# Performance work log

Hardware: AMD Instinct MI355X
Metric: run time of the kernel (lower is better)

The kernel has to match this reference:

```python
import jax, jax.numpy as jnp
import numpy as np

B, S, D = 2, 2048, 1024
H, DH = 16, 64  # num_heads, qk/vo embed size per head
NEG_INF = -1e9


def setup_inputs() -> dict:
    key = jax.random.key(0)
    ks = jax.random.split(key, 7)
    return {
        "query": jax.random.normal(ks[0], (B, S, D), jnp.float32),
        "key": jax.random.normal(ks[1], (B, S, D), jnp.float32),
        "value": jax.random.normal(ks[2], (B, S, D), jnp.float32),
        "Wq": jax.random.normal(ks[3], (D, D), jnp.float32) * 0.02,
        "Wk": jax.random.normal(ks[4], (D, D), jnp.float32) * 0.02,
        "Wv": jax.random.normal(ks[5], (D, D), jnp.float32) * 0.02,
        "Wo": jax.random.normal(ks[6], (D, D), jnp.float32) * 0.02,
    }


def reference(query, key, value, Wq, Wk, Wv, Wo):
    # projections (nn.Linear, no bias): y = x @ W.T
    q = (query @ Wq.T).reshape(B, S, H, DH)
    k = (key @ Wk.T).reshape(B, S, H, DH)
    v = (value @ Wv.T).reshape(B, S, H, DH)
    # scores normalized by sqrt(per-head qk embed dim)
    scores = jnp.einsum("bqhd,bkhd->bhqk", q, k) / jnp.sqrt(jnp.float32(DH))
    # causal mask
    causal = jnp.tril(jnp.ones((S, S), dtype=bool))
    scores = jnp.where(causal[None, None, :, :], scores, NEG_INF)
    attn = jax.nn.softmax(scores, axis=-1)  # attention_type='softmax'
    ctx = jnp.einsum("bhqk,bkhd->bqhd", attn, v).reshape(B, S, H * DH)
    return ctx @ Wo.T
```

## Files before the change

### kernel.cpp

```cpp
#include <hip/hip_runtime.h>
#include <hip/hip_bf16.h>
#include <cstdint>


typedef __attribute__((ext_vector_type(8))) __bf16 bf16x8;
typedef __attribute__((ext_vector_type(8))) unsigned short ushort8;
typedef __attribute__((ext_vector_type(4))) unsigned short usv4;
typedef __attribute__((ext_vector_type(4))) float f32x4;
typedef unsigned short ushort_t;

#define B_ 2
#define S_ 2048
#define D_ 1024
#define H_ 16
#define DH_ 64
#define BK 64

#define QSCALE 0.1803368801111244f

__device__ __forceinline__ ushort_t f2b(float f) {
  uint32_t u = __builtin_bit_cast(uint32_t, f);
  u += 0x7fffu + ((u >> 16) & 1u);
  return (ushort_t)(u >> 16);
}
__device__ __forceinline__ ushort_t f2bf(float f) {
  uint32_t u = __builtin_bit_cast(uint32_t, f);
  return (ushort_t)((u + 0x8000u) >> 16);
}

__device__ __forceinline__ f32x4 mfma16(bf16x8 a, bf16x8 b, f32x4 c) {
  return __builtin_amdgcn_mfma_f32_16x16x32_bf16(a, b, c, 0, 0, 0);
}

__device__ __forceinline__ void gload16(const ushort_t* g, char* lds) {
  __builtin_amdgcn_global_load_lds(
      (__attribute__((address_space(1))) void*)(uintptr_t)g,
      (__attribute__((address_space(3))) void*)(uintptr_t)lds, 16, 0, 0);
}

__global__ __launch_bounds__(256) void cvt3_kernel(
    const float* __restrict__ s0, const float* __restrict__ s1,
    const float* __restrict__ s2, ushort_t* __restrict__ d0,
    ushort_t* __restrict__ d1, ushort_t* __restrict__ d2) {
  const float* src = blockIdx.y == 0 ? s0 : (blockIdx.y == 1 ? s1 : s2);
  ushort_t* dst = blockIdx.y == 0 ? d0 : (blockIdx.y == 1 ? d1 : d2);
  int i = blockIdx.x * 256 + threadIdx.x;
  f32x4 a = ((const f32x4*)src)[i * 2];
  f32x4 b = ((const f32x4*)src)[i * 2 + 1];
  ushort8 o;
#pragma unroll
  for (int j = 0; j < 4; ++j) o[j] = f2b(a[j]);
#pragma unroll
  for (int j = 0; j < 4; ++j) o[4 + j] = f2b(b[j]);
  ((ushort8*)dst)[i] = o;
}

__global__ __launch_bounds__(256) void cvt4_kernel(
    const float* __restrict__ s0, const float* __restrict__ s1,
    const float* __restrict__ s2, const float* __restrict__ s3,
    ushort_t* __restrict__ d0, ushort_t* __restrict__ d1,
    ushort_t* __restrict__ d2, ushort_t* __restrict__ d3) {
  const float* src = blockIdx.y == 0 ? s0
                     : (blockIdx.y == 1 ? s1 : (blockIdx.y == 2 ? s2 : s3));
  ushort_t* dst = blockIdx.y == 0 ? d0
                  : (blockIdx.y == 1 ? d1 : (blockIdx.y == 2 ? d2 : d3));
  int i = blockIdx.x * 256 + threadIdx.x;
  f32x4 a = ((const f32x4*)src)[i * 2];
  f32x4 b = ((const f32x4*)src)[i * 2 + 1];
  ushort8 o;
#pragma unroll
  for (int j = 0; j < 4; ++j) o[j] = f2b(a[j]);
#pragma unroll
  for (int j = 0; j < 4; ++j) o[4 + j] = f2b(b[j]);
  ((ushort8*)dst)[i] = o;
}

template <int TBM, int TBN, int OUTF32>
__device__ __forceinline__ void gemm_body(const ushort_t* __restrict__ A,
                                          const ushort_t* __restrict__ W,
                                          void* __restrict__ Cout,
                                          int M, int N, int K, float scale,
                                          int i0, int j0) {
  constexpr int MI = TBM / 32, NJ = TBN / 32;
  __shared__ char smem[(TBM + TBN) * BK * 2];
  char* sA = smem;
  char* sB = smem + TBM * BK * 2;
  const int tid = threadIdx.x;
  const int w = tid >> 6, lane = tid & 63, l16 = lane & 15, lg = lane >> 4;
  const int wr = (w >> 1) * (TBM / 2), wc = (w & 1) * (TBN / 2);
  f32x4 acc[MI][NJ] = {};
  const int nk = K / BK;
  for (int kt = 0; kt < nk; ++kt) {
    const int k0 = kt * BK;
    __syncthreads();
#pragma unroll
    for (int is = 0; is < MI; ++is) {
      int chunk = is * 256 + tid;
      int row = chunk >> 3, s = chunk & 7, sl = s ^ (row & 7);
      gload16(A + (size_t)(i0 + row) * K + k0 + sl * 8, sA + (is * 4 + w) * 1024);
    }
#pragma unroll
    for (int is = 0; is < NJ; ++is) {
      int chunk = is * 256 + tid;
      int row = chunk >> 3, s = chunk & 7, sl = s ^ (row & 7);
      gload16(W + (size_t)(j0 + row) * K + k0 + sl * 8, sB + (is * 4 + w) * 1024);
    }
    __syncthreads();
#pragma unroll
    for (int ks = 0; ks < 2; ++ks) {
      bf16x8 af[MI], bfr[NJ];
#pragma unroll
      for (int mi = 0; mi < MI; ++mi) {
        int r = wr + mi * 16 + l16;
        af[mi] = *(const bf16x8*)(sA + r * 128 + ((ks * 64 + lg * 16) ^ ((r & 7) << 4)));
      }
#pragma unroll
      for (int nj = 0; nj < NJ; ++nj) {
        int r = wc + nj * 16 + l16;
        bfr[nj] = *(const bf16x8*)(sB + r * 128 + ((ks * 64 + lg * 16) ^ ((r & 7) << 4)));
      }
#pragma unroll
      for (int mi = 0; mi < MI; ++mi)
#pragma unroll
        for (int nj = 0; nj < NJ; ++nj)
          acc[mi][nj] = mfma16(af[mi], bfr[nj], acc[mi][nj]);
    }
  }
#pragma unroll
  for (int mi = 0; mi < MI; ++mi)
#pragma unroll
    for (int nj = 0; nj < NJ; ++nj)
#pragma unroll
      for (int r = 0; r < 4; ++r) {
        int row = i0 + wr + mi * 16 + lg * 4 + r;
        int col = j0 + wc + nj * 16 + l16;
        float v = acc[mi][nj][r] * scale;
        if (OUTF32)
          ((float*)Cout)[(size_t)row * N + col] = v;
        else
          ((ushort_t*)Cout)[(size_t)row * N + col] = f2b(v);
      }
}

template <int TBM, int TBN, int OUTF32>
__device__ __forceinline__ void gemm_db(const ushort_t* __restrict__ A,
                                        const ushort_t* __restrict__ W,
                                        void* __restrict__ Cout,
                                        int M, int N, int K, float scale,
                                        int i0, int j0) {
  constexpr int MI = TBM / 32, NJ = TBN / 32;
  constexpr int BUFB = (TBM + TBN) * BK * 2;
  __shared__ char smem[2 * BUFB];
  const int tid = threadIdx.x;
  const int w = tid >> 6, lane = tid & 63, l16 = lane & 15, lg = lane >> 4;
  const int wr = (w >> 1) * (TBM / 2), wc = (w & 1) * (TBN / 2);
  f32x4 acc[MI][NJ] = {};
  const int nk = K / BK;

  auto stage = [&](int kt, int buf) {
    char* sA = smem + buf * BUFB;
    char* sB = sA + TBM * BK * 2;
    const int k0 = kt * BK;
#pragma unroll
    for (int is = 0; is < MI; ++is) {
      int chunk = is * 256 + tid;
      int row = chunk >> 3, s = chunk & 7, sl = s ^ (row & 7);
      gload16(A + (size_t)(i0 + row) * K + k0 + sl * 8, sA + (is * 4 + w) * 1024);
    }
#pragma unroll
    for (int is = 0; is < NJ; ++is) {
      int chunk = is * 256 + tid;
      int row = chunk >> 3, s = chunk & 7, sl = s ^ (row & 7);
      gload16(W + (size_t)(j0 + row) * K + k0 + sl * 8, sB + (is * 4 + w) * 1024);
    }
  };

  stage(0, 0);
  __syncthreads();
  int cur = 0;
  for (int kt = 0; kt < nk; ++kt) {
    if (kt + 1 < nk) stage(kt + 1, cur ^ 1);
    char* sA = smem + cur * BUFB;
    char* sB = sA + TBM * BK * 2;
#pragma unroll
    for (int ks = 0; ks < 2; ++ks) {
      bf16x8 af[MI], bfr[NJ];
#pragma unroll
      for (int mi = 0; mi < MI; ++mi) {
        int r = wr + mi * 16 + l16;
        af[mi] = *(const bf16x8*)(sA + r * 128 + ((ks * 64 + lg * 16) ^ ((r & 7) << 4)));
      }
#pragma unroll
      for (int nj = 0; nj < NJ; ++nj) {
        int r = wc + nj * 16 + l16;
        bfr[nj] = *(const bf16x8*)(sB + r * 128 + ((ks * 64 + lg * 16) ^ ((r & 7) << 4)));
      }
#pragma unroll
      for (int mi = 0; mi < MI; ++mi)
#pragma unroll
        for (int nj = 0; nj < NJ; ++nj)
          acc[mi][nj] = mfma16(af[mi], bfr[nj], acc[mi][nj]);
    }
    __syncthreads();
    cur ^= 1;
  }
#pragma unroll
  for (int mi = 0; mi < MI; ++mi)
#pragma unroll
    for (int nj = 0; nj < NJ; ++nj)
#pragma unroll
      for (int r = 0; r < 4; ++r) {
        int row = i0 + wr + mi * 16 + lg * 4 + r;
        int col = j0 + wc + nj * 16 + l16;
        float v = acc[mi][nj][r] * scale;
        if (OUTF32)
          ((float*)Cout)[(size_t)row * N + col] = v;
        else
          ((ushort_t*)Cout)[(size_t)row * N + col] = f2b(v);
      }
}

__global__ __launch_bounds__(256) void qkv_gemm(
    const ushort_t* __restrict__ xq, const ushort_t* __restrict__ xk,
    const ushort_t* __restrict__ xv, const ushort_t* __restrict__ wq,
    const ushort_t* __restrict__ wk, const ushort_t* __restrict__ wv,
    ushort_t* __restrict__ Qb, ushort_t* __restrict__ Kb,
    ushort_t* __restrict__ Vt) {
  const int z = blockIdx.z;
  if (z < 2) {
    gemm_body<128, 128, 0>(z ? xk : xq, z ? wk : wq, z ? Kb : Qb,
                           B_ * S_, D_, D_, z ? 1.f : QSCALE,
                           blockIdx.x * 128, blockIdx.y * 128);
  } else {
    gemm_body<128, 128, 0>(wv, xv, Vt, D_, B_ * S_, D_, 1.f,
                           blockIdx.y * 128, blockIdx.x * 128);
  }
}

__global__ __launch_bounds__(256) void out_gemm(const ushort_t* __restrict__ ctx,
                                                const ushort_t* __restrict__ wo,
                                                float* __restrict__ out) {
  gemm_db<128, 64, 1>(ctx, wo, out, B_ * S_, D_, D_, 1.f,
                      blockIdx.y * 128, blockIdx.x * 64);
}

__global__ __launch_bounds__(256) void attn_kernel(
    const ushort_t* __restrict__ Qb, const ushort_t* __restrict__ Kb,
    const ushort_t* __restrict__ VtG, ushort_t* __restrict__ ctx) {
  const int bh = blockIdx.x;
  const int pair = blockIdx.y;
  const int b = bh >> 4, h = bh & 15;
  const int tid = threadIdx.x;
  const int w = tid >> 6, lane = tid & 63, l16 = lane & 15, lg = lane >> 4;

  __shared__ char smem[2 * 16384 + 4 * 2048];
  char* sP = smem + 32768 + w * 2048;

  const size_t BS = (size_t)B_ * S_;
  const size_t qkbase = ((size_t)b * S_) * D_ + h * DH_;
  const ushort_t* Vbase = VtG + (size_t)(h * 64) * BS + (size_t)b * S_;

  const int srow = tid >> 3, sslot = (tid & 7) ^ (srow & 7);
  const size_t koff0 = (size_t)srow * D_ + sslot * 8;
  const size_t koff1 = koff0 + (size_t)32 * D_;
  const size_t voff0 = (size_t)srow * BS + sslot * 8;
  const size_t voff1 = voff0 + (size_t)32 * BS;
  const int dst0 = w * 1024, dst1 = 4096 + w * 1024;

  const int pwsw = (l16 & 7) << 4;
  const int pbase = l16 * 128;

  for (int sub = 0; sub < 2; ++sub) {
    const int qt = sub ? (31 - pair) : pair;
    const int q0 = qt * 64 + w * 16;
    const int qg0 = q0 + l16;
    const int tl = qt;

    bf16x8 qf[2];
    {
      const ushort_t* qrow = Qb + qkbase + (size_t)qg0 * D_;
      qf[0] = *(const bf16x8*)(qrow + lg * 8);
      qf[1] = *(const bf16x8*)(qrow + 32 + lg * 8);
    }

    f32x4 acc_o[4] = {};
    float m = -1e30f, lsum = 0.f;

    int cur = 0;
    {
      const ushort_t* Ksrc = Kb + qkbase;
      gload16(Ksrc + koff0, smem + dst0);
      gload16(Ksrc + koff1, smem + dst1);
      gload16(Vbase + voff0, smem + 8192 + dst0);
      gload16(Vbase + voff1, smem + 8192 + dst1);
    }
    __syncthreads();

    for (int t = 0; t <= tl; ++t) {
      if (t < tl) {
        char* bK = smem + (cur ^ 1) * 16384;
        const ushort_t* Ksrc = Kb + qkbase + (size_t)((t + 1) * 64) * D_;
        const ushort_t* Vsrc = Vbase + (t + 1) * 64;
        gload16(Ksrc + koff0, bK + dst0);
        gload16(Ksrc + koff1, bK + dst1);
        gload16(Vsrc + voff0, bK + 8192 + dst0);
        gload16(Vsrc + voff1, bK + 8192 + dst1);
      }
      char* bK = smem + cur * 16384;
      char* bV = bK + 8192;

      f32x4 sc[4] = {};
      __builtin_amdgcn_s_setprio(1);
#pragma unroll
      for (int ks = 0; ks < 2; ++ks)
#pragma unroll
        for (int nt = 0; nt < 4; ++nt) {
          int rk = nt * 16 + l16;
          bf16x8 kf = *(const bf16x8*)(bK + rk * 128 + ((ks * 64 + lg * 16) ^ ((rk & 7) << 4)));
          sc[nt] = mfma16(kf, qf[ks], sc[nt]);
        }
      __builtin_amdgcn_s_setprio(0);
      if (t == tl) {
#pragma unroll
        for (int nt = 0; nt < 4; ++nt)
#pragma unroll
          for (int r = 0; r < 4; ++r) {
            int kg = t * 64 + nt * 16 + lg * 4 + r;
            if (kg > qg0) sc[nt][r] = -1e30f;
          }
      }
      float v = sc[0][0];
#pragma unroll
      for (int nt = 0; nt < 4; ++nt)
#pragma unroll
        for (int r = 0; r < 4; ++r) v = fmaxf(v, sc[nt][r]);
      v = fmaxf(v, __shfl_xor(v, 16));
      v = fmaxf(v, __shfl_xor(v, 32));
      if (!__all(v <= m)) {
        float mn = fmaxf(m, v);
        float alpha = exp2f(m - mn);
        m = mn;
        lsum *= alpha;
#pragma unroll
        for (int r = 0; r < 4; ++r) {
          float ar = __shfl(alpha, lg * 4 + r);
#pragma unroll
          for (int nt = 0; nt < 4; ++nt) acc_o[nt][r] *= ar;
        }
      }
      float rs = 0.f;
#pragma unroll
      for (int nt = 0; nt < 4; ++nt) {
        usv4 pk;
#pragma unroll
        for (int r = 0; r < 4; ++r) {
          float p = exp2f(sc[nt][r] - m);
          rs += p;
          pk[r] = f2bf(p);
        }
        *(usv4*)(sP + pbase + ((nt * 32 + lg * 8) ^ pwsw)) = pk;
      }
      rs += __shfl_xor(rs, 16);
      rs += __shfl_xor(rs, 32);
      lsum += rs;
      __builtin_amdgcn_s_setprio(1);
#pragma unroll
      for (int ks = 0; ks < 2; ++ks) {
        bf16x8 pa = *(const bf16x8*)(sP + pbase + ((ks * 64 + lg * 16) ^ pwsw));
#pragma unroll
        for (int nt = 0; nt < 4; ++nt) {
          int dr = nt * 16 + l16;
          bf16x8 vb = *(const bf16x8*)(bV + dr * 128 + ((ks * 64 + lg * 16) ^ ((dr & 7) << 4)));
          acc_o[nt] = mfma16(pa, vb, acc_o[nt]);
        }
      }
      __builtin_amdgcn_s_setprio(0);
      __syncthreads();
      cur ^= 1;
    }
#pragma unroll
    for (int r = 0; r < 4; ++r) {
      float inv = 1.f / __shfl(lsum, lg * 4 + r);
      int qg = q0 + lg * 4 + r;
      ushort_t* crow = ctx + qkbase + (size_t)qg * D_;
#pragma unroll
      for (int nt = 0; nt < 4; ++nt) crow[nt * 16 + l16] = f2b(acc_o[nt][r] * inv);
    }
  }
}

extern "C" void kernel_launch(void* const* d_in, const int* in_sizes, int n_in,
                              void* d_out, int out_size, void* d_ws, size_t ws_size,
                              hipStream_t stream) {
  const float* query = (const float*)d_in[0];
  const float* key   = (const float*)d_in[1];
  const float* value = (const float*)d_in[2];
  const float* Wq    = (const float*)d_in[3];
  const float* Wk    = (const float*)d_in[4];
  const float* Wv    = (const float*)d_in[5];
  const float* Wo    = (const float*)d_in[6];

  char* ws = (char*)d_ws;
  const size_t SZ = (size_t)B_ * S_ * D_ * 2;
  const size_t WSZ = (size_t)D_ * D_ * 2;
  ushort_t* xq  = (ushort_t*)(ws + 0 * SZ);
  ushort_t* xk  = (ushort_t*)(ws + 1 * SZ);
  ushort_t* xv  = (ushort_t*)(ws + 2 * SZ);
  ushort_t* Qb  = (ushort_t*)(ws + 3 * SZ);
  ushort_t* Kb  = (ushort_t*)(ws + 4 * SZ);
  ushort_t* Vt  = (ushort_t*)(ws + 5 * SZ);
  ushort_t* ctx = xq;
  ushort_t* wqb = (ushort_t*)(ws + 6 * SZ + 0 * WSZ);
  ushort_t* wkb = (ushort_t*)(ws + 6 * SZ + 1 * WSZ);
  ushort_t* wvb = (ushort_t*)(ws + 6 * SZ + 2 * WSZ);
  ushort_t* wob = (ushort_t*)(ws + 6 * SZ + 3 * WSZ);

  const int n8a = B_ * S_ * D_ / 8;
  const int n8w = D_ * D_ / 8;
  cvt3_kernel<<<dim3(n8a / 256, 3), 256, 0, stream>>>(query, key, value, xq, xk, xv);
  cvt4_kernel<<<dim3(n8w / 256, 4), 256, 0, stream>>>(Wq, Wk, Wv, Wo, wqb, wkb, wvb, wob);

  qkv_gemm<<<dim3(32, 8, 3), 256, 0, stream>>>(xq, xk, xv, wqb, wkb, wvb, Qb, Kb, Vt);

  attn_kernel<<<dim3(B_ * H_, 16), 256, 0, stream>>>(Qb, Kb, Vt, ctx);

  out_gemm<<<dim3(D_ / 64, (B_ * S_) / 128), 256, 0, stream>>>(ctx, wob, (float*)d_out);
}
```

Measured before the change: 217.5 us.

## Merge conversion kernels and streamline attention softmax inner loop

Merges the two fp32-to-bf16 conversion launches into one kernel to save a launch and its tail. In the attention loop it uses incremental K/V pointers, a tree-shaped max reduction, and a lazy max-rescale threshold of 8 (in log2 units), so the accumulator is rescaled only when the running max grows by more than that. Probabilities are now computed into an array, summed with a tree, and converted with the native bf16 cast. The lazy rescale lets exponentials reach up to 2^8 before rescaling, which trades rare rescale work for a small risk to precision and overflow.

```diff
diff --git a/kernel.cpp b/kernel.cpp
--- a/kernel.cpp
+++ b/kernel.cpp
@@ -4,8 +4,8 @@
 
 
 typedef __attribute__((ext_vector_type(8))) __bf16 bf16x8;
+typedef __attribute__((ext_vector_type(4))) __bf16 bf16x4;
 typedef __attribute__((ext_vector_type(8))) unsigned short ushort8;
-typedef __attribute__((ext_vector_type(4))) unsigned short usv4;
 typedef __attribute__((ext_vector_type(4))) float f32x4;
 typedef unsigned short ushort_t;
 
@@ -23,10 +23,6 @@
   u += 0x7fffu + ((u >> 16) & 1u);
   return (ushort_t)(u >> 16);
 }
-__device__ __forceinline__ ushort_t f2bf(float f) {
-  uint32_t u = __builtin_bit_cast(uint32_t, f);
-  return (ushort_t)((u + 0x8000u) >> 16);
-}
 
 __device__ __forceinline__ f32x4 mfma16(bf16x8 a, bf16x8 b, f32x4 c) {
   return __builtin_amdgcn_mfma_f32_16x16x32_bf16(a, b, c, 0, 0, 0);
@@ -38,33 +34,30 @@
       (__attribute__((address_space(3))) void*)(uintptr_t)lds, 16, 0, 0);
 }
 
-__global__ __launch_bounds__(256) void cvt3_kernel(
-    const float* __restrict__ s0, const float* __restrict__ s1,
-    const float* __restrict__ s2, ushort_t* __restrict__ d0,
-    ushort_t* __restrict__ d1, ushort_t* __restrict__ d2) {
-  const float* src = blockIdx.y == 0 ? s0 : (blockIdx.y == 1 ? s1 : s2);
-  ushort_t* dst = blockIdx.y == 0 ? d0 : (blockIdx.y == 1 ? d1 : d2);
-  int i = blockIdx.x * 256 + threadIdx.x;
-  f32x4 a = ((const f32x4*)src)[i * 2];
-  f32x4 b = ((const f32x4*)src)[i * 2 + 1];
-  ushort8 o;
-#pragma unroll
-  for (int j = 0; j < 4; ++j) o[j] = f2b(a[j]);
-#pragma unroll
-  for (int j = 0; j < 4; ++j) o[4 + j] = f2b(b[j]);
-  ((ushort8*)dst)[i] = o;
-}
-
-__global__ __launch_bounds__(256) void cvt4_kernel(
-    const float* __restrict__ s0, const float* __restrict__ s1,
-    const float* __restrict__ s2, const float* __restrict__ s3,
-    ushort_t* __restrict__ d0, ushort_t* __restrict__ d1,
-    ushort_t* __restrict__ d2, ushort_t* __restrict__ d3) {
-  const float* src = blockIdx.y == 0 ? s0
-                     : (blockIdx.y == 1 ? s1 : (blockIdx.y == 2 ? s2 : s3));
-  ushort_t* dst = blockIdx.y == 0 ? d0
-                  : (blockIdx.y == 1 ? d1 : (blockIdx.y == 2 ? d2 : d3));
-  int i = blockIdx.x * 256 + threadIdx.x;
+__global__ __launch_bounds__(256) void cvt_all(
+    const float* __restrict__ q, const float* __restrict__ k,
+    const float* __restrict__ v, const float* __restrict__ wq,
+    const float* __restrict__ wk, const float* __restrict__ wv,
+    const float* __restrict__ wo, ushort_t* __restrict__ dq,
+    ushort_t* __restrict__ dk, ushort_t* __restrict__ dv,
+    ushort_t* __restrict__ dwq, ushort_t* __restrict__ dwk,
+    ushort_t* __restrict__ dwv, ushort_t* __restrict__ dwo) {
+  const int gid = blockIdx.x;
+  const float* src;
+  ushort_t* dst;
+  int i;
+  if (gid < 6144) {
+    int t = gid >> 11;
+    src = t == 0 ? q : (t == 1 ? k : v);
+    dst = t == 0 ? dq : (t == 1 ? dk : dv);
+    i = (gid & 2047) * 256 + threadIdx.x;
+  } else {
+    int g = gid - 6144;
+    int t = g >> 9;
+    src = t == 0 ? wq : (t == 1 ? wk : (t == 2 ? wv : wo));
+    dst = t == 0 ? dwq : (t == 1 ? dwk : (t == 2 ? dwv : dwo));
+    i = (g & 511) * 256 + threadIdx.x;
+  }
   f32x4 a = ((const f32x4*)src)[i * 2];
   f32x4 b = ((const f32x4*)src)[i * 2 + 1];
   ushort8 o;
@@ -296,15 +289,17 @@
     }
     __syncthreads();
 
+    const ushort_t* Kst = Kb + qkbase + (size_t)64 * D_;
+    const ushort_t* Vst = Vbase + 64;
     for (int t = 0; t <= tl; ++t) {
       if (t < tl) {
         char* bK = smem + (cur ^ 1) * 16384;
-        const ushort_t* Ksrc = Kb + qkbase + (size_t)((t + 1) * 64) * D_;
-        const ushort_t* Vsrc = Vbase + (t + 1) * 64;
-        gload16(Ksrc + koff0, bK + dst0);
-        gload16(Ksrc + koff1, bK + dst1);
-        gload16(Vsrc + voff0, bK + 8192 + dst0);
-        gload16(Vsrc + voff1, bK + 8192 + dst1);
+        gload16(Kst + koff0, bK + dst0);
+        gload16(Kst + koff1, bK + dst1);
+        gload16(Vst + voff0, bK + 8192 + dst0);
+        gload16(Vst + voff1, bK + 8192 + dst1);
+        Kst += (size_t)64 * D_;
+        Vst += 64;
       }
       char* bK = smem + cur * 16384;
       char* bV = bK + 8192;
@@ -329,14 +324,15 @@
             if (kg > qg0) sc[nt][r] = -1e30f;
           }
       }
-      float v = sc[0][0];
-#pragma unroll
-      for (int nt = 0; nt < 4; ++nt)
-#pragma unroll
-        for (int r = 0; r < 4; ++r) v = fmaxf(v, sc[nt][r]);
+      float a0 = fmaxf(fmaxf(sc[0][0], sc[0][1]), sc[0][2]);
+      float a1 = fmaxf(fmaxf(sc[0][3], sc[1][0]), sc[1][1]);
+      float a2 = fmaxf(fmaxf(sc[1][2], sc[1][3]), sc[2][0]);
+      float a3 = fmaxf(fmaxf(sc[2][1], sc[2][2]), sc[2][3]);
+      float a4 = fmaxf(fmaxf(sc[3][0], sc[3][1]), sc[3][2]);
+      float v = fmaxf(fmaxf(fmaxf(a0, a1), fmaxf(a2, a3)), fmaxf(a4, sc[3][3]));
       v = fmaxf(v, __shfl_xor(v, 16));
       v = fmaxf(v, __shfl_xor(v, 32));
-      if (!__all(v <= m)) {
+      if (!__all(v <= m + 8.f)) {
         float mn = fmaxf(m, v);
         float alpha = exp2f(m - mn);
         m = mn;
@@ -348,18 +344,22 @@
           for (int nt = 0; nt < 4; ++nt) acc_o[nt][r] *= ar;
         }
       }
-      float rs = 0.f;
+      float pe[4][4];
+#pragma unroll
+      for (int nt = 0; nt < 4; ++nt)
+#pragma unroll
+        for (int r = 0; r < 4; ++r) pe[nt][r] = exp2f(sc[nt][r] - m);
 #pragma unroll
       for (int nt = 0; nt < 4; ++nt) {
-        usv4 pk;
-#pragma unroll
-        for (int r = 0; r < 4; ++r) {
-          float p = exp2f(sc[nt][r] - m);
-          rs += p;
-          pk[r] = f2bf(p);
-        }
-        *(usv4*)(sP + pbase + ((nt * 32 + lg * 8) ^ pwsw)) = pk;
-      }
+        bf16x4 pk;
+#pragma unroll
+        for (int r = 0; r < 4; ++r) pk[r] = (__bf16)pe[nt][r];
+        *(bf16x4*)(sP + pbase + ((nt * 32 + lg * 8) ^ pwsw)) = pk;
+      }
+      float rs = ((pe[0][0] + pe[0][1]) + (pe[0][2] + pe[0][3]))
+               + ((pe[1][0] + pe[1][1]) + (pe[1][2] + pe[1][3]));
+      rs += ((pe[2][0] + pe[2][1]) + (pe[2][2] + pe[2][3]))
+          + ((pe[3][0] + pe[3][1]) + (pe[3][2] + pe[3][3]));
       rs += __shfl_xor(rs, 16);
       rs += __shfl_xor(rs, 32);
       lsum += rs;
@@ -415,10 +415,8 @@
   ushort_t* wvb = (ushort_t*)(ws + 6 * SZ + 2 * WSZ);
   ushort_t* wob = (ushort_t*)(ws + 6 * SZ + 3 * WSZ);
 
-  const int n8a = B_ * S_ * D_ / 8;
-  const int n8w = D_ * D_ / 8;
-  cvt3_kernel<<<dim3(n8a / 256, 3), 256, 0, stream>>>(query, key, value, xq, xk, xv);
-  cvt4_kernel<<<dim3(n8w / 256, 4), 256, 0, stream>>>(Wq, Wk, Wv, Wo, wqb, wkb, wvb, wob);
+  cvt_all<<<8192, 256, 0, stream>>>(query, key, value, Wq, Wk, Wv, Wo,
+                                    xq, xk, xv, wqb, wkb, wvb, wob);
 
   qkv_gemm<<<dim3(32, 8, 3), 256, 0, stream>>>(xq, xk, xv, wqb, wkb, wvb, Qb, Kb, Vt);
 
```

Result: no change. 213.7 us (-1.8%).
